# Optimization experiments

Measured on AMD Instinct MI355X. Metric: run time of the kernel, lower is better.

## Reference

```python
import jax, jax.numpy as jnp
import numpy as np

B, S, HID = 2, 2048, 2048
H, HKV = 16, 4
D = HID // H          # 128
N_REP = H // HKV      # 4
ROPE_THETA = 1000000.0


def _rope_tables(seq_len, head_dim, theta):
    inv_freq = 1.0 / (theta ** (jnp.arange(0, head_dim, 2, dtype=jnp.float32) / head_dim))
    freqs = jnp.arange(seq_len, dtype=jnp.float32)[:, None] * inv_freq[None, :]  # [S, D/2]
    emb = jnp.concatenate([freqs, freqs], axis=-1)  # [S, D]
    return jnp.cos(emb), jnp.sin(emb)


def setup_inputs() -> dict:
    key = jax.random.key(0)
    ks = jax.random.split(key, 6)
    cos, sin = _rope_tables(S, D, ROPE_THETA)
    sc = 0.02
    return {
        "x": jax.random.normal(ks[0], (B, S, HID), jnp.float32),
        "cos": cos,
        "sin": sin,
        "Wq": jax.random.normal(ks[1], (HID, H * D), jnp.float32) * sc,
        "Wk": jax.random.normal(ks[2], (HID, HKV * D), jnp.float32) * sc,
        "Wv": jax.random.normal(ks[3], (HID, HKV * D), jnp.float32) * sc,
        "Wo": jax.random.normal(ks[4], (H * D, HID), jnp.float32) * sc,
    }


def _rotate_half(t):
    t1, t2 = jnp.split(t, 2, axis=-1)
    return jnp.concatenate([-t2, t1], axis=-1)


def reference(x, cos, sin, Wq, Wk, Wv, Wo):
    b, s, _ = x.shape
    q = (x @ Wq).reshape(b, s, H, D)    # [b,s,H,d]
    k = (x @ Wk).reshape(b, s, HKV, D)  # [b,s,Hkv,d]
    v = (x @ Wv).reshape(b, s, HKV, D)

    # RoPE (cos/sin broadcast over head axis)
    c = cos[:s, None, :]  # [s,1,d]
    sn = sin[:s, None, :]
    q = q * c + _rotate_half(q) * sn
    k = k * c + _rotate_half(k) * sn

    # GQA: repeat kv heads (interleaved, matching repeat_kv)
    k = jnp.repeat(k, N_REP, axis=2)  # [b,s,H,d]
    v = jnp.repeat(v, N_REP, axis=2)

    q = q.transpose(0, 2, 1, 3)  # [b,H,s,d]
    k = k.transpose(0, 2, 1, 3)
    v = v.transpose(0, 2, 1, 3)

    scale = 1.0 / jnp.sqrt(jnp.asarray(D, x.dtype))
    scores = jnp.einsum("bhqd,bhkd->bhqk", q, k) * scale
    causal = jnp.tril(jnp.ones((s, s), dtype=bool))
    scores = jnp.where(causal[None, None], scores, jnp.asarray(-jnp.inf, scores.dtype))
    probs = jax.nn.softmax(scores, axis=-1)
    out = jnp.einsum("bhqk,bhkd->bhqd", probs, v)
    out = out.transpose(0, 2, 1, 3).reshape(b, s, H * D)
    return out @ Wo
```

## Files before the change

### kernel.cpp

```cpp
#include <hip/hip_runtime.h>
#include <cstdint>

#define B_    2
#define S_    2048
#define HID_  2048
#define H_    16
#define HKV_  4
#define D_    128
#define SCALE_ 0.08838834764831845f
#define LOG2E_ 1.4426950408889634f
#define K1_   (SCALE_ * LOG2E_)
#define THRS_ 62.75f

typedef __bf16 bf16x8 __attribute__((ext_vector_type(8)));
typedef float  f32x4  __attribute__((ext_vector_type(4)));
using u16 = unsigned short;

static __device__ __forceinline__ u16 f2bf(float f) {
  union { float f; uint32_t u; } c; c.f = f;
  uint32_t u = c.u;
  return (u16)((u + 0x7FFFu + ((u >> 16) & 1u)) >> 16);
}
static __device__ __forceinline__ float bf2f(u16 h) {
  union { uint32_t u; float f; } c; c.u = ((uint32_t)h) << 16;
  return c.f;
}
static __device__ __forceinline__ void async16(const u16* g, u16* lds) {
  __builtin_amdgcn_global_load_lds((const __attribute__((address_space(1))) void*)g,
                                   (__attribute__((address_space(3))) void*)lds, 16, 0, 0);
}

__global__ __launch_bounds__(256) void prep_cast_weights(const float* __restrict__ x,
                                                         const float* __restrict__ Wq,
                                                         const float* __restrict__ Wk,
                                                         const float* __restrict__ Wv,
                                                         const float* __restrict__ Wo,
                                                         u16* __restrict__ xb,
                                                         u16* __restrict__ Wt,
                                                         u16* __restrict__ Wot) {
  __shared__ float tile[32][33];
  const int t = blockIdx.x;
  const int tid = threadIdx.x;
  if (t < 8192) {
    const int i = t * 256 + tid;
    float4 v = ((const float4*)x)[i];
    ushort4 o;
    o.x = f2bf(v.x); o.y = f2bf(v.y); o.z = f2bf(v.z); o.w = f2bf(v.w);
    ((ushort4*)xb)[i] = o;
    return;
  }
  const int tw = t - 8192;
  const float* W; u16* Dst; int N, lt;
  if (tw < 4096)      { W = Wq; Dst = Wt;                        N = 2048; lt = tw; }
  else if (tw < 5120) { W = Wk; Dst = Wt + (size_t)2048 * 2048;  N = 512;  lt = tw - 4096; }
  else if (tw < 6144) { W = Wv; Dst = Wt + (size_t)2560 * 2048;  N = 512;  lt = tw - 5120; }
  else                { W = Wo; Dst = Wot;                       N = 2048; lt = tw - 6144; }
  const int tx = tid & 31, ty = tid >> 5;
  const int tn = N >> 5;
  const int n0 = (lt % tn) * 32, k0 = (lt / tn) * 32;
#pragma unroll
  for (int j = 0; j < 32; j += 8)
    tile[ty + j][tx] = W[(size_t)(k0 + ty + j) * N + n0 + tx];
  __syncthreads();
#pragma unroll
  for (int j = 0; j < 32; j += 8)
    Dst[(size_t)(n0 + ty + j) * 2048 + k0 + tx] = f2bf(tile[tx][ty + j]);
}

__global__ __launch_bounds__(256) void prep_rope_k(const u16* __restrict__ qkv,
                                                   const float* __restrict__ cosb,
                                                   const float* __restrict__ sinb,
                                                   u16* __restrict__ Kr) {
  const int idx = blockIdx.x * 256 + threadIdx.x;
  const int j = (idx & 31) * 2, rest = idx >> 5;
  const int kv = rest & 3, srow = rest >> 2;
  const int s = srow & (S_ - 1);
  const u16* base = qkv + (size_t)srow * 3072 + 2048 + kv * 128;
  const float2 cc = *(const float2*)&cosb[s * 128 + j];
  const float2 ss = *(const float2*)&sinb[s * 128 + j];
  const ushort2 av = *(const ushort2*)&base[j];
  const ushort2 bv = *(const ushort2*)&base[j + 64];
  const float a0 = bf2f(av.x), a1 = bf2f(av.y);
  const float b0 = bf2f(bv.x), b1 = bf2f(bv.y);
  const size_t ko = (((size_t)(srow >> 11) * HKV_ + kv) * S_ + s) * D_;
  ushort2 lo, hi;
  lo.x = f2bf(a0 * cc.x - b0 * ss.x); lo.y = f2bf(a1 * cc.y - b1 * ss.y);
  hi.x = f2bf(b0 * cc.x + a0 * ss.x); hi.y = f2bf(b1 * cc.y + a1 * ss.y);
  *(ushort2*)&Kr[ko + j]      = lo;
  *(ushort2*)&Kr[ko + j + 64] = hi;
}

template<int MODE>
__global__ __launch_bounds__(256, 3) void gemm_bt(const u16* __restrict__ A,
                                                  const u16* __restrict__ Bt,
                                                  void* __restrict__ Cv,
                                                  u16* __restrict__ Vt,
                                                  int M, int N, int K, int gx) {
  const int nwg = (int)gridDim.x;
  const int bid = (int)blockIdx.x;
  const int qq = nwg >> 3, rr = nwg & 7;
  const int xcd = bid & 7, pos = bid >> 3;
  const int wg = ((xcd < rr) ? xcd * (qq + 1) : rr * (qq + 1) + (xcd - rr) * qq) + pos;
  const int bm = (wg % gx) * 128;
  const int bn = (wg / gx) * 128;

  __shared__ __align__(16) u16 Ash[128 * 64];
  __shared__ __align__(16) u16 Bsh[128 * 64];
  const int tid = threadIdx.x;
  const int w = tid >> 6, l = tid & 63;
  const int wm = (w >> 1) * 64, wn = (w & 1) * 64;

  const f32x4 z4 = {0.f, 0.f, 0.f, 0.f};
  f32x4 acc[4][4];
#pragma unroll
  for (int i = 0; i < 4; ++i)
#pragma unroll
    for (int j = 0; j < 4; ++j) acc[i][j] = z4;

  const int srow = w * 8 + (l >> 3);
  const int schunk = l & 7;

  for (int k0 = 0; k0 < K; k0 += 64) {
#pragma unroll
    for (int i = 0; i < 4; ++i) {
      const int row = i * 32 + srow;
      const int ch = schunk ^ (row & 7);
      async16(A + (size_t)(bm + row) * K + k0 + ch * 8, &Ash[(i * 4 + w) * 512]);
      async16(Bt + (size_t)(bn + row) * K + k0 + ch * 8, &Bsh[(i * 4 + w) * 512]);
    }
    asm volatile("s_waitcnt vmcnt(0)" ::: "memory");
    __syncthreads();
#pragma unroll
    for (int kc = 0; kc < 2; ++kc) {
      bf16x8 af[4], bfr[4];
#pragma unroll
      for (int mi = 0; mi < 4; ++mi) {
        const int r = wm + mi * 16 + (l & 15);
        const int c2 = (kc * 4 + (l >> 4)) ^ (r & 7);
        af[mi] = *(const bf16x8*)&Ash[r * 64 + c2 * 8];
      }
#pragma unroll
      for (int ni = 0; ni < 4; ++ni) {
        const int r = wn + ni * 16 + (l & 15);
        const int c2 = (kc * 4 + (l >> 4)) ^ (r & 7);
        bfr[ni] = *(const bf16x8*)&Bsh[r * 64 + c2 * 8];
      }
#pragma unroll
      for (int mi = 0; mi < 4; ++mi)
#pragma unroll
        for (int ni = 0; ni < 4; ++ni)
          acc[mi][ni] = __builtin_amdgcn_mfma_f32_16x16x32_bf16(af[mi], bfr[ni], acc[mi][ni], 0, 0, 0);
    }
    __syncthreads();
  }

  if (MODE == 1 && bn >= 2560) {
    const int kv = (bn - 2560) >> 7;
#pragma unroll
    for (int mi = 0; mi < 4; ++mi) {
      const int r0 = bm + wm + mi * 16 + ((l >> 4) << 2);
      const int bb = r0 >> 11;
      const int s0 = r0 & (S_ - 1);
      const int a  = (s0 & 63) >> 2;
      const int pb = ((a >> 3) * 4 + (a & 3)) * 8 + ((a >> 2) & 1) * 4;
      const int spb = (s0 & ~63) | pb;
      u16* vb = Vt + ((size_t)(bb * HKV_ + kv) * D_) * S_ + spb;
#pragma unroll
      for (int ni = 0; ni < 4; ++ni) {
        const int d = wn + ni * 16 + (l & 15);
        ushort4 o;
        o.x = f2bf(acc[mi][ni][0]); o.y = f2bf(acc[mi][ni][1]);
        o.z = f2bf(acc[mi][ni][2]); o.w = f2bf(acc[mi][ni][3]);
        *(ushort4*)&vb[(size_t)d * S_] = o;
      }
    }
  } else {
#pragma unroll
    for (int mi = 0; mi < 4; ++mi) {
      const int r0 = bm + wm + mi * 16 + ((l >> 4) << 2);
#pragma unroll
      for (int ni = 0; ni < 4; ++ni) {
        const int c = bn + wn + ni * 16 + (l & 15);
#pragma unroll
        for (int j = 0; j < 4; ++j) {
          if (MODE == 1) ((u16*)Cv)[(size_t)(r0 + j) * N + c] = f2bf(acc[mi][ni][j]);
          else           ((float*)Cv)[(size_t)(r0 + j) * N + c] = acc[mi][ni][j];
        }
      }
    }
  }
}

__global__ __launch_bounds__(256, 3) void attn_kernel(const u16* __restrict__ qkv,
                                                      const float* __restrict__ cosb,
                                                      const float* __restrict__ sinb,
                                                      const u16* __restrict__ Kc,
                                                      const u16* __restrict__ Vt,
                                                      u16* __restrict__ O) {
  const int bid = blockIdx.x;
  const int p   = bid & 7;
  const int hs  = (bid >> 3) & 3;
  const int idx = bid >> 5;
  const int grp = idx >> 3, jj2 = idx & 7;
  const int qt  = (grp == 0) ? (31 - jj2) : (grp == 1) ? jj2
                : (grp == 2) ? (23 - jj2) : (8 + jj2);
  const int b   = p >> 2;
  const int kvh = p & 3;
  const int h   = kvh * 4 + hs;
  const int tid = threadIdx.x;
  const int w = tid >> 6, l = tid & 63;
  const int g = l >> 4, c = l & 15;
  const int q0 = qt * 64;

  __shared__ __align__(16) u16 Ksh[64 * 128];
  __shared__ __align__(16) u16 VshF[2 * 128 * 64];

  const u16* Kbase = Kc + ((size_t)(b * HKV_ + kvh) * S_) * D_;
  const u16* Vbase = Vt + ((size_t)(b * HKV_ + kvh) * D_) * S_;

  bf16x8 qf[4];
  {
    const int s_q = q0 + w * 16 + c;
    const u16* qp = qkv + (size_t)(b * S_ + s_q) * 3072 + h * 128 + g * 8;
    bf16x8 qraw[4];
#pragma unroll
    for (int kc = 0; kc < 4; ++kc) qraw[kc] = *(const bf16x8*)(qp + kc * 32);
    const float* cp = cosb + s_q * 128 + g * 8;
    const float* sp = sinb + s_q * 128 + g * 8;
#pragma unroll
    for (int kcp = 0; kcp < 2; ++kcp) {
      float cl[8], sl[8];
      *(float4*)&cl[0] = *(const float4*)(cp + kcp * 32);
      *(float4*)&cl[4] = *(const float4*)(cp + kcp * 32 + 4);
      *(float4*)&sl[0] = *(const float4*)(sp + kcp * 32);
      *(float4*)&sl[4] = *(const float4*)(sp + kcp * 32 + 4);
      bf16x8 lo, hi;
#pragma unroll
      for (int j = 0; j < 8; ++j) {
        const float a  = (float)qraw[kcp][j];
        const float b2 = (float)qraw[kcp + 2][j];
        lo[j] = (__bf16)(a * cl[j] - b2 * sl[j]);
        hi[j] = (__bf16)(b2 * cl[j] + a * sl[j]);
      }
      qf[kcp] = lo; qf[kcp + 2] = hi;
    }
  }

  int srcK[4], srcV[4];
#pragma unroll
  for (int i = 0; i < 4; ++i) {
    const int rK = i * 16 + w * 4 + g;
    srcK[i] = rK * 128 + (c ^ (rK & 7)) * 8;
    const int dV = i * 32 + w * 8 + (l >> 3);
    srcV[i] = dV * S_ + ((l & 7) ^ (dV & 7)) * 8;
  }

  const f32x4 z4 = {0.f, 0.f, 0.f, 0.f};
  f32x4 oacc[8];
#pragma unroll
  for (int nb = 0; nb < 8; ++nb) oacc[nb] = z4;
  float m_i = -1e30f, l_i = 0.f;

  auto stageK = [&](int kv0) {
#pragma unroll
    for (int i = 0; i < 4; ++i)
      async16(Kbase + (size_t)kv0 * 128 + srcK[i], &Ksh[i * 2048 + w * 512]);
  };
  auto stageV = [&](int buf, int kv0) {
#pragma unroll
    for (int i = 0; i < 4; ++i)
      async16(Vbase + kv0 + srcV[i], &VshF[buf * 8192 + i * 2048 + w * 512]);
  };

  const int nt = qt + 1;
  stageV(0, 0);
  stageK(0);

  for (int t = 0; t < nt; ++t) {
    const int cur = t & 1;
    asm volatile("s_waitcnt vmcnt(0)" ::: "memory");
    __syncthreads();
    if (t + 1 < nt) stageV(cur ^ 1, (t + 1) << 6);

    f32x4 sf[4];
#pragma unroll
    for (int nb = 0; nb < 4; ++nb) sf[nb] = z4;

    __builtin_amdgcn_s_setprio(1);
#pragma unroll
    for (int kc = 0; kc < 4; ++kc) {
#pragma unroll
      for (int nb = 0; nb < 4; ++nb) {
        const int r = nb * 16 + c;
        const int s2 = (kc * 4 + g) ^ (c & 7);
        const bf16x8 kf = *(const bf16x8*)&Ksh[r * 128 + s2 * 8];
        sf[nb] = __builtin_amdgcn_mfma_f32_16x16x32_bf16(kf, qf[kc], sf[nb], 0, 0, 0);
      }
    }
    __builtin_amdgcn_s_setprio(0);

    __syncthreads();
    if (t + 1 < nt) stageK((t + 1) << 6);

    {
      const int kv0 = t << 6;
      const int qcol = q0 + w * 16 + c;
      const bool doMask = (t == nt - 1);
      float mx = -3e38f;
#pragma unroll
      for (int nb = 0; nb < 4; ++nb)
#pragma unroll
        for (int jj = 0; jj < 4; ++jj) {
          float sv = sf[nb][jj];
          if (doMask) {
            const int kk = kv0 + nb * 16 + g * 4 + jj;
            sv = (kk > qcol) ? -3e38f : sv;
            sf[nb][jj] = sv;
          }
          mx = fmaxf(mx, sv);
        }
      mx = fmaxf(mx, __shfl_xor(mx, 16));
      mx = fmaxf(mx, __shfl_xor(mx, 32));

      if (__all(mx <= m_i + THRS_)) {
        const float mk = m_i * K1_;
        float rs = 0.f;
#pragma unroll
        for (int nb = 0; nb < 4; ++nb)
#pragma unroll
          for (int jj = 0; jj < 4; ++jj) {
            const float p2 = exp2f(fmaf(sf[nb][jj], K1_, -mk));
            sf[nb][jj] = p2;
            rs += p2;
          }
        rs += __shfl_xor(rs, 16);
        rs += __shfl_xor(rs, 32);
        l_i += rs;
      } else {
        const float mnew = fmaxf(m_i, mx);
        const float fsc = exp2f((m_i - mnew) * K1_);
        m_i = mnew;
        const float mk = mnew * K1_;
        float rs = 0.f;
#pragma unroll
        for (int nb = 0; nb < 4; ++nb)
#pragma unroll
          for (int jj = 0; jj < 4; ++jj) {
            const float p2 = exp2f(fmaf(sf[nb][jj], K1_, -mk));
            sf[nb][jj] = p2;
            rs += p2;
          }
        rs += __shfl_xor(rs, 16);
        rs += __shfl_xor(rs, 32);
        l_i = l_i * fsc + rs;
        float fq[4];
#pragma unroll
        for (int j = 0; j < 4; ++j) fq[j] = __shfl(fsc, g * 4 + j);
#pragma unroll
        for (int nb = 0; nb < 8; ++nb)
#pragma unroll
          for (int j = 0; j < 4; ++j) oacc[nb][j] *= fq[j];
      }
    }

    bf16x8 pa, pb;
#pragma unroll
    for (int jj = 0; jj < 4; ++jj) {
      pa[jj] = (__bf16)sf[0][jj]; pa[4 + jj] = (__bf16)sf[1][jj];
      pb[jj] = (__bf16)sf[2][jj]; pb[4 + jj] = (__bf16)sf[3][jj];
    }

    const char* Vb = (const char*)&VshF[cur * 8192] + c * 128;
    __builtin_amdgcn_s_setprio(1);
#pragma unroll
    for (int kc2 = 0; kc2 < 2; ++kc2) {
      const bf16x8 pfr = kc2 ? pb : pa;
      const int s2v = ((kc2 * 4 + g) ^ (c & 7)) << 4;
#pragma unroll
      for (int nb = 0; nb < 8; ++nb) {
        const bf16x8 vf = *(const bf16x8*)(Vb + nb * 2048 + s2v);
        oacc[nb] = __builtin_amdgcn_mfma_f32_16x16x32_bf16(pfr, vf, oacc[nb], 0, 0, 0);
      }
    }
    __builtin_amdgcn_s_setprio(0);
  }

#pragma unroll
  for (int j = 0; j < 4; ++j) {
    const float li = __shfl(l_i, g * 4 + j);
    const float inv = 1.f / li;
    const int srow = q0 + w * 16 + g * 4 + j;
    u16* op = O + ((size_t)(b * S_ + srow)) * HID_ + h * D_ + c;
#pragma unroll
    for (int nb = 0; nb < 8; ++nb) op[nb * 16] = f2bf(oacc[nb][j] * inv);
  }
}

extern "C" void kernel_launch(void* const* d_in, const int* in_sizes, int n_in,
                              void* d_out, int out_size, void* d_ws, size_t ws_size,
                              hipStream_t stream) {
  const float* x    = (const float*)d_in[0];
  const float* cosb = (const float*)d_in[1];
  const float* sinb = (const float*)d_in[2];
  const float* Wq   = (const float*)d_in[3];
  const float* Wk   = (const float*)d_in[4];
  const float* Wv   = (const float*)d_in[5];
  const float* Wo   = (const float*)d_in[6];
  float* out = (float*)d_out;

  u16*   xb   = (u16*)d_ws;
  u16*   Wt   = xb  + (size_t)4096 * 2048;
  u16*   Wot  = Wt  + (size_t)3072 * 2048;
  u16*   qkv  = Wot + (size_t)2048 * 2048;
  u16*   Kr   = qkv + (size_t)4096 * 3072;
  u16*   Vtb  = Kr  + (size_t)B_ * HKV_ * S_ * D_;
  u16*   Ob   = Vtb + (size_t)B_ * HKV_ * S_ * D_;

  prep_cast_weights<<<dim3(18432), 256, 0, stream>>>(x, Wq, Wk, Wv, Wo, xb, Wt, Wot);

  gemm_bt<1><<<dim3(768), 256, 0, stream>>>(xb, Wt, qkv, Vtb, 4096, 3072, 2048, 32);

  prep_rope_k<<<dim3(2048), 256, 0, stream>>>(qkv, cosb, sinb, Kr);

  attn_kernel<<<dim3(1024), 256, 0, stream>>>(qkv, cosb, sinb, Kr, Vtb, Ob);

  gemm_bt<0><<<dim3(512), 256, 0, stream>>>(Ob, Wot, out, nullptr, 4096, 2048, 2048, 32);
}
```

Measured before the change: 195.9 us.

## Halve attention KV tile to 32, skip fully masked waves, stage Q via LDS

The attention kernel now walks the keys in 32-row tiles instead of 64, with smaller K/V shared buffers and a new V swizzle, and raises the launch bound to 4 blocks per CU. Each wave skips the QK, softmax and PV work for tiles lying entirely above its causal diagonal, which cuts wasted work on the diagonal tile. Q is loaded coalesced through shared memory before RoPE instead of read per lane from global. The cost is twice as many loop iterations, each with two barriers, and less MFMA work per synchronisation.

```diff
diff --git a/kernel.cpp b/kernel.cpp
--- a/kernel.cpp
+++ b/kernel.cpp
@@ -191,7 +191,7 @@
   }
 }
 
-__global__ __launch_bounds__(256, 3) void attn_kernel(const u16* __restrict__ qkv,
+__global__ __launch_bounds__(256, 4) void attn_kernel(const u16* __restrict__ qkv,
                                                       const float* __restrict__ cosb,
                                                       const float* __restrict__ sinb,
                                                       const u16* __restrict__ Kc,
@@ -212,19 +212,30 @@
   const int g = l >> 4, c = l & 15;
   const int q0 = qt * 64;
 
-  __shared__ __align__(16) u16 Ksh[64 * 128];
-  __shared__ __align__(16) u16 VshF[2 * 128 * 64];
+  __shared__ __align__(16) u16 Qsh[64 * 128];
+  __shared__ __align__(16) u16 Ksh[32 * 128];
+  __shared__ __align__(16) u16 VshF[2 * 128 * 32];
 
   const u16* Kbase = Kc + ((size_t)(b * HKV_ + kvh) * S_) * D_;
   const u16* Vbase = Vt + ((size_t)(b * HKV_ + kvh) * D_) * S_;
 
   bf16x8 qf[4];
   {
-    const int s_q = q0 + w * 16 + c;
-    const u16* qp = qkv + (size_t)(b * S_ + s_q) * 3072 + h * 128 + g * 8;
+    const u16* Qb = qkv + ((size_t)b * S_ + q0) * 3072 + h * 128;
+#pragma unroll
+    for (int i = 0; i < 4; ++i) {
+      const int rQ = i * 16 + (tid >> 4);
+      async16(Qb + (size_t)rQ * 3072 + ((tid & 15) ^ (rQ & 7)) * 8, &Qsh[(i * 256 + tid) * 8]);
+    }
+    asm volatile("s_waitcnt vmcnt(0)" ::: "memory");
+    __builtin_amdgcn_sched_barrier(0);
+    __builtin_amdgcn_s_barrier();
+    const int rr = w * 16 + c;
+    const int s_q = q0 + rr;
     bf16x8 qraw[4];
 #pragma unroll
-    for (int kc = 0; kc < 4; ++kc) qraw[kc] = *(const bf16x8*)(qp + kc * 32);
+    for (int kc = 0; kc < 4; ++kc)
+      qraw[kc] = *(const bf16x8*)&Qsh[rr * 128 + ((kc * 4 + g) ^ (c & 7)) * 8];
     const float* cp = cosb + s_q * 128 + g * 8;
     const float* sp = sinb + s_q * 128 + g * 8;
 #pragma unroll
@@ -246,13 +257,13 @@
     }
   }
 
-  int srcK[4], srcV[4];
-#pragma unroll
-  for (int i = 0; i < 4; ++i) {
-    const int rK = i * 16 + w * 4 + g;
-    srcK[i] = rK * 128 + (c ^ (rK & 7)) * 8;
-    const int dV = i * 32 + w * 8 + (l >> 3);
-    srcV[i] = dV * S_ + ((l & 7) ^ (dV & 7)) * 8;
+  int srcK[2], srcV[2];
+#pragma unroll
+  for (int i = 0; i < 2; ++i) {
+    const int rK = i * 16 + (tid >> 4);
+    srcK[i] = rK * 128 + ((tid & 15) ^ (rK & 7)) * 8;
+    const int dV = i * 64 + (tid >> 2);
+    srcV[i] = dV * S_ + (((tid & 3) ^ ((dV >> 1) & 3))) * 8;
   }
 
   const f32x4 z4 = {0.f, 0.f, 0.f, 0.f};
@@ -263,126 +274,126 @@
 
   auto stageK = [&](int kv0) {
 #pragma unroll
-    for (int i = 0; i < 4; ++i)
-      async16(Kbase + (size_t)kv0 * 128 + srcK[i], &Ksh[i * 2048 + w * 512]);
+    for (int i = 0; i < 2; ++i)
+      async16(Kbase + (size_t)kv0 * 128 + srcK[i], &Ksh[(i * 256 + tid) * 8]);
   };
   auto stageV = [&](int buf, int kv0) {
 #pragma unroll
-    for (int i = 0; i < 4; ++i)
-      async16(Vbase + kv0 + srcV[i], &VshF[buf * 8192 + i * 2048 + w * 512]);
+    for (int i = 0; i < 2; ++i)
+      async16(Vbase + kv0 + srcV[i], &VshF[buf * 4096 + (i * 256 + tid) * 8]);
   };
 
-  const int nt = qt + 1;
+  const uint32_t voff = (uint32_t)(c * 64 + ((g ^ ((c >> 1) & 3)) << 4));
+
+  const int nt = 2 * (qt + 1);
   stageV(0, 0);
   stageK(0);
 
   for (int t = 0; t < nt; ++t) {
     const int cur = t & 1;
+    const int kv0 = t << 5;
     asm volatile("s_waitcnt vmcnt(0)" ::: "memory");
     __syncthreads();
-    if (t + 1 < nt) stageV(cur ^ 1, (t + 1) << 6);
-
-    f32x4 sf[4];
-#pragma unroll
-    for (int nb = 0; nb < 4; ++nb) sf[nb] = z4;
-
-    __builtin_amdgcn_s_setprio(1);
-#pragma unroll
-    for (int kc = 0; kc < 4; ++kc) {
-#pragma unroll
-      for (int nb = 0; nb < 4; ++nb) {
-        const int r = nb * 16 + c;
-        const int s2 = (kc * 4 + g) ^ (c & 7);
-        const bf16x8 kf = *(const bf16x8*)&Ksh[r * 128 + s2 * 8];
-        sf[nb] = __builtin_amdgcn_mfma_f32_16x16x32_bf16(kf, qf[kc], sf[nb], 0, 0, 0);
-      }
-    }
-    __builtin_amdgcn_s_setprio(0);
+    if (t + 1 < nt) stageV(cur ^ 1, (t + 1) << 5);
+
+    const bool live = (kv0 <= q0 + w * 16 + 15);
+
+    f32x4 sf[2];
+    sf[0] = z4; sf[1] = z4;
+    if (live) {
+      __builtin_amdgcn_s_setprio(1);
+#pragma unroll
+      for (int kc = 0; kc < 4; ++kc) {
+#pragma unroll
+        for (int nb = 0; nb < 2; ++nb) {
+          const int r = nb * 16 + c;
+          const int s2 = (kc * 4 + g) ^ (c & 7);
+          const bf16x8 kf = *(const bf16x8*)&Ksh[r * 128 + s2 * 8];
+          sf[nb] = __builtin_amdgcn_mfma_f32_16x16x32_bf16(kf, qf[kc], sf[nb], 0, 0, 0);
+        }
+      }
+      __builtin_amdgcn_s_setprio(0);
+    }
 
     __syncthreads();
-    if (t + 1 < nt) stageK((t + 1) << 6);
-
-    {
-      const int kv0 = t << 6;
-      const int qcol = q0 + w * 16 + c;
-      const bool doMask = (t == nt - 1);
-      float mx = -3e38f;
-#pragma unroll
-      for (int nb = 0; nb < 4; ++nb)
-#pragma unroll
-        for (int jj = 0; jj < 4; ++jj) {
-          float sv = sf[nb][jj];
-          if (doMask) {
-            const int kk = kv0 + nb * 16 + g * 4 + jj;
-            sv = (kk > qcol) ? -3e38f : sv;
-            sf[nb][jj] = sv;
+    if (t + 1 < nt) stageK((t + 1) << 5);
+
+    if (live) {
+      {
+        const int qcol = q0 + w * 16 + c;
+        const bool doMask = (kv0 + 31 > q0 + w * 16);
+        float mx = -3e38f;
+#pragma unroll
+        for (int nb = 0; nb < 2; ++nb)
+#pragma unroll
+          for (int jj = 0; jj < 4; ++jj) {
+            float sv = sf[nb][jj];
+            if (doMask) {
+              const int kk = kv0 + nb * 16 + g * 4 + jj;
+              sv = (kk > qcol) ? -3e38f : sv;
+              sf[nb][jj] = sv;
+            }
+            mx = fmaxf(mx, sv);
           }
-          mx = fmaxf(mx, sv);
+        mx = fmaxf(mx, __shfl_xor(mx, 16));
+        mx = fmaxf(mx, __shfl_xor(mx, 32));
+
+        if (__all(mx <= m_i + THRS_)) {
+          const float mk = m_i * K1_;
+          float rs = 0.f;
+#pragma unroll
+          for (int nb = 0; nb < 2; ++nb)
+#pragma unroll
+            for (int jj = 0; jj < 4; ++jj) {
+              const float p2 = exp2f(fmaf(sf[nb][jj], K1_, -mk));
+              sf[nb][jj] = p2;
+              rs += p2;
+            }
+          rs += __shfl_xor(rs, 16);
+          rs += __shfl_xor(rs, 32);
+          l_i += rs;
+        } else {
+          const float mnew = fmaxf(m_i, mx);
+          const float fsc = exp2f((m_i - mnew) * K1_);
+          m_i = mnew;
+          const float mk = mnew * K1_;
+          float rs = 0.f;
+#pragma unroll
+          for (int nb = 0; nb < 2; ++nb)
+#pragma unroll
+            for (int jj = 0; jj < 4; ++jj) {
+              const float p2 = exp2f(fmaf(sf[nb][jj], K1_, -mk));
+              sf[nb][jj] = p2;
+              rs += p2;
+            }
+          rs += __shfl_xor(rs, 16);
+          rs += __shfl_xor(rs, 32);
+          l_i = l_i * fsc + rs;
+          float fq[4];
+#pragma unroll
+          for (int j = 0; j < 4; ++j) fq[j] = __shfl(fsc, g * 4 + j);
+#pragma unroll
+          for (int nb = 0; nb < 8; ++nb)
+#pragma unroll
+            for (int j = 0; j < 4; ++j) oacc[nb][j] *= fq[j];
         }
-      mx = fmaxf(mx, __shfl_xor(mx, 16));
-      mx = fmaxf(mx, __shfl_xor(mx, 32));
-
-      if (__all(mx <= m_i + THRS_)) {
-        const float mk = m_i * K1_;
-        float rs = 0.f;
-#pragma unroll
-        for (int nb = 0; nb < 4; ++nb)
-#pragma unroll
-          for (int jj = 0; jj < 4; ++jj) {
-            const float p2 = exp2f(fmaf(sf[nb][jj], K1_, -mk));
-            sf[nb][jj] = p2;
-            rs += p2;
-          }
-        rs += __shfl_xor(rs, 16);
-        rs += __shfl_xor(rs, 32);
-        l_i += rs;
-      } else {
-        const float mnew = fmaxf(m_i, mx);
-        const float fsc = exp2f((m_i - mnew) * K1_);
-        m_i = mnew;
-        const float mk = mnew * K1_;
-        float rs = 0.f;
-#pragma unroll
-        for (int nb = 0; nb < 4; ++nb)
-#pragma unroll
-          for (int jj = 0; jj < 4; ++jj) {
-            const float p2 = exp2f(fmaf(sf[nb][jj], K1_, -mk));
-            sf[nb][jj] = p2;
-            rs += p2;
-          }
-        rs += __shfl_xor(rs, 16);
-        rs += __shfl_xor(rs, 32);
-        l_i = l_i * fsc + rs;
-        float fq[4];
-#pragma unroll
-        for (int j = 0; j < 4; ++j) fq[j] = __shfl(fsc, g * 4 + j);
-#pragma unroll
-        for (int nb = 0; nb < 8; ++nb)
-#pragma unroll
-          for (int j = 0; j < 4; ++j) oacc[nb][j] *= fq[j];
-      }
-    }
-
-    bf16x8 pa, pb;
-#pragma unroll
-    for (int jj = 0; jj < 4; ++jj) {
-      pa[jj] = (__bf16)sf[0][jj]; pa[4 + jj] = (__bf16)sf[1][jj];
-      pb[jj] = (__bf16)sf[2][jj]; pb[4 + jj] = (__bf16)sf[3][jj];
-    }
-
-    const char* Vb = (const char*)&VshF[cur * 8192] + c * 128;
-    __builtin_amdgcn_s_setprio(1);
-#pragma unroll
-    for (int kc2 = 0; kc2 < 2; ++kc2) {
-      const bf16x8 pfr = kc2 ? pb : pa;
-      const int s2v = ((kc2 * 4 + g) ^ (c & 7)) << 4;
+      }
+
+      bf16x8 pa;
+#pragma unroll
+      for (int jj = 0; jj < 4; ++jj) {
+        pa[jj] = (__bf16)sf[0][jj]; pa[4 + jj] = (__bf16)sf[1][jj];
+      }
+
+      const char* Vb = (const char*)&VshF[cur * 4096] + voff;
+      __builtin_amdgcn_s_setprio(1);
 #pragma unroll
       for (int nb = 0; nb < 8; ++nb) {
-        const bf16x8 vf = *(const bf16x8*)(Vb + nb * 2048 + s2v);
-        oacc[nb] = __builtin_amdgcn_mfma_f32_16x16x32_bf16(pfr, vf, oacc[nb], 0, 0, 0);
-      }
-    }
-    __builtin_amdgcn_s_setprio(0);
+        const bf16x8 vf = *(const bf16x8*)(Vb + nb * 1024);
+        oacc[nb] = __builtin_amdgcn_mfma_f32_16x16x32_bf16(pa, vf, oacc[nb], 0, 0, 0);
+      }
+      __builtin_amdgcn_s_setprio(0);
+    }
   }
 
 #pragma unroll
```

Measured after the change: 205.7 us. 5.0% more time.
